# Kernel tuning notes

Hardware: AMD Instinct MI355X
Metric: run time of the kernel (lower is better)

Reference implementation:

```python
import jax, jax.numpy as jnp
import numpy as np

EPS_BN = 1e-5
EPS_LN = 1e-5

def _bn(x, g, b, m, v):
    # inference-mode BatchNorm2d over channel dim 1
    scale = g / jnp.sqrt(v + EPS_BN)
    return x * scale[None, :, None, None] + (b - m * scale)[None, :, None, None]

def _conv1x1(x, w, b=None):
    y = jnp.einsum('bchw,oc->bohw', x, w)
    if b is not None:
        y = y + b[None, :, None, None]
    return y

def _gelu(x):
    return jax.nn.gelu(x, approximate=False)

def setup_inputs() -> dict:
    key = jax.random.key(0)
    ks = jax.random.split(key, 40)
    B, C, H, W = 32, 160, 56, 56
    C5, C3 = C // 5, C * 3
    s = 0.05
    d = {}
    d['x'] = jax.random.normal(ks[0], (B, C, H, W), jnp.float32)
    d['bn1_g'] = jax.random.uniform(ks[1], (C,), jnp.float32, 0.5, 1.5)
    d['bn1_b'] = jax.random.normal(ks[2], (C,)) * s
    d['bn1_m'] = jax.random.normal(ks[3], (C,)) * s
    d['bn1_v'] = jnp.ones((C,), jnp.float32)
    names = ['t', 'b', 'r', 'l', 'c']
    for i, n in enumerate(names):
        d['w' + n] = jax.random.normal(ks[4 + i], (C5, C)) * s
        d['b' + n] = jax.random.normal(ks[9 + i], (C5,)) * s
    d['wf1'] = jax.random.normal(ks[14], (C, C)) * s
    d['bf1'] = jax.random.normal(ks[15], (C,)) * s
    d['bn2_g'] = jax.random.uniform(ks[16], (C,), jnp.float32, 0.5, 1.5)
    d['bn2_b'] = jax.random.normal(ks[17], (C,)) * s
    d['bn2_m'] = jax.random.normal(ks[18], (C,)) * s
    d['bn2_v'] = jnp.ones((C,), jnp.float32)
    d['wph'] = jax.random.normal(ks[19], (W, W)) * s
    d['bph'] = jax.random.normal(ks[20], (W,)) * s
    d['wpw'] = jax.random.normal(ks[21], (H, H)) * s
    d['bpw'] = jax.random.normal(ks[22], (H,)) * s
    d['wf2'] = jax.random.normal(ks[23], (C, C3)) * s
    d['ln_g'] = jax.random.uniform(ks[24], (C,), jnp.float32, 0.5, 1.5)
    d['ln_b'] = jax.random.normal(ks[25], (C,)) * s
    d['wfc1'] = jax.random.normal(ks[26], (C3, C)) * s
    d['bfc1'] = jax.random.normal(ks[27], (C3,)) * s
    d['wfc2'] = jax.random.normal(ks[28], (C, C3)) * s
    d['bfc2'] = jax.random.normal(ks[29], (C,)) * s
    d['step'] = 1
    return d

def reference(x, bn1_g, bn1_b, bn1_m, bn1_v, wt, bt, wb, bb, wr, br, wl, bl, wc, bc,
              wf1, bf1, bn2_g, bn2_b, bn2_m, bn2_v, wph, bph, wpw, bpw, wf2,
              ln_g, ln_b, wfc1, bfc1, wfc2, bfc2, step):
    B, C, H, W = x.shape
    # ---- localMix: ShiftedPillarsConcatentation_BNAct_NP5 ----
    h = _gelu(_bn(x, bn1_g, bn1_b, bn1_m, bn1_v))
    x_t = _conv1x1(h, wt, bt)
    x_b = _conv1x1(h, wb, bb)
    x_r = _conv1x1(h, wr, br)
    x_l = _conv1x1(h, wl, bl)
    x_c = _conv1x1(h, wc, bc)
    # pad then narrow exactly as torch: t/l shift by 1, b/r shift by step
    x_t = jnp.pad(x_t, ((0, 0), (0, 0), (0, step), (0, 0)))[:, :, 1:1 + H, :]
    x_b = jnp.pad(x_b, ((0, 0), (0, 0), (step, 0), (0, 0)))[:, :, 0:H, :]
    x_l = jnp.pad(x_l, ((0, 0), (0, 0), (0, 0), (0, step)))[:, :, :, 1:1 + W]
    x_r = jnp.pad(x_r, ((0, 0), (0, 0), (0, 0), (step, 0)))[:, :, :, 0:W]
    lm = _conv1x1(jnp.concatenate([x_t, x_b, x_r, x_l, x_c], axis=1), wf1, bf1)
    # ---- globalMix: sparseMLP_BNAct ----
    g = _gelu(_bn(lm, bn2_g, bn2_b, bn2_m, bn2_v))
    # proj_h mixes the W axis (input permuted to (B,W,C,H)), bias per output W
    x_h = jnp.einsum('bchw,vw->bchv', g, wph) + bph[None, None, None, :]
    # proj_w mixes the H axis (input permuted to (B,H,C,W)), bias per output H
    x_w = jnp.einsum('bchw,uh->bcuw', g, wpw) + bpw[None, None, :, None]
    gm = _conv1x1(jnp.concatenate([g, x_h, x_w], axis=1), wf2)  # no bias
    x1 = gm + x  # residual 1
    # ---- channelMix: LN + Mlp over channels ----
    y = jnp.transpose(x1, (0, 2, 3, 1))  # BHWC
    mu = jnp.mean(y, axis=-1, keepdims=True)
    var = jnp.mean(jnp.square(y - mu), axis=-1, keepdims=True)
    y = (y - mu) / jnp.sqrt(var + EPS_LN) * ln_g + ln_b
    y = _gelu(jnp.einsum('bhwc,fc->bhwf', y, wfc1) + bfc1)
    y = jnp.einsum('bhwf,cf->bhwc', y, wfc2) + bfc2
    return jnp.transpose(y, (0, 3, 1, 2)) + x1  # residual 2
```

## Files before the change

kernel.cpp:

```cpp
#include <hip/hip_runtime.h>
#include <hip/hip_bf16.h>
#include <math.h>

typedef __hip_bfloat16 bf16;
typedef __attribute__((ext_vector_type(8))) short s8v;
typedef __attribute__((ext_vector_type(4))) float f4v;

#define Bn  32
#define Cn  160
#define HWn 3136
#define Pn  100352

__device__ __forceinline__ float b2f(bf16 v){ return __bfloat162float(v); }
__device__ __forceinline__ bf16  f2b(float v){ return __float2bfloat16(v); }
__device__ __forceinline__ float bits2f(unsigned short u){
    union { float f; unsigned int i; } x; x.i = ((unsigned int)u) << 16; return x.f;
}
__device__ __forceinline__ float gelu_f(float x){ return 0.5f*x*(1.0f + erff(x*0.7071067811865476f)); }

#define MFMA(a,b,c) __builtin_amdgcn_mfma_f32_16x16x32_bf16((a),(b),(c),0,0,0)

__global__ __launch_bounds__(256) void k0_prep(
    const float* __restrict__ wt, const float* __restrict__ wb_, const float* __restrict__ wr,
    const float* __restrict__ wl, const float* __restrict__ wc,
    const float* __restrict__ bt, const float* __restrict__ bb_, const float* __restrict__ br,
    const float* __restrict__ bl, const float* __restrict__ bc,
    const float* __restrict__ wf1, const float* __restrict__ bf1,
    const float* __restrict__ g2, const float* __restrict__ b2, const float* __restrict__ m2, const float* __restrict__ v2,
    const float* __restrict__ wf2, const float* __restrict__ wfc1, const float* __restrict__ wfc2,
    const float* __restrict__ wph, const float* __restrict__ wpw,
    bf16* wcat, bf16* wf1b, bf16* wf2b, bf16* wfc1b, bf16* wfc2b, bf16* wphb, bf16* wpwb,
    float* bcat, float* epsv, float* eptv)
{
    int idx = blockIdx.x*256 + threadIdx.x;
    if (idx < 25600){ int o = idx/160, k = idx - o*160; int gi = o>>5, oo = o&31;
        const float* wp = gi==0?wt: gi==1?wb_: gi==2?wr: gi==3?wl: wc;
        wcat[idx] = f2b(wp[oo*160+k]); return; }
    idx -= 25600;
    if (idx < 25600){ wf1b[idx] = f2b(wf1[idx]); return; }
    idx -= 25600;
    if (idx < 76800){ wf2b[idx] = f2b(wf2[idx]); return; }
    idx -= 76800;
    if (idx < 76800){ wfc1b[idx] = f2b(wfc1[idx]); return; }
    idx -= 76800;
    if (idx < 76800){ wfc2b[idx] = f2b(wfc2[idx]); return; }
    idx -= 76800;
    if (idx < 4096){ int v = idx>>6, w = idx&63;
        wphb[idx] = (v<56 && w<56) ? f2b(wph[v*56+w]) : f2b(0.f); return; }
    idx -= 4096;
    if (idx < 4096){ int v = idx>>6, w = idx&63;
        wpwb[idx] = (v<56 && w<56) ? f2b(wpw[v*56+w]) : f2b(0.f); return; }
    idx -= 4096;
    if (idx < 160){ int o = idx; int gi = o>>5, oo = o&31;
        const float* bp = gi==0?bt: gi==1?bb_: gi==2?br: gi==3?bl: bc;
        bcat[o] = bp[oo]; return; }
    idx -= 160;
    if (idx < 160){ int o = idx; float s = g2[o]*rsqrtf(v2[o]+1e-5f);
        epsv[o] = s; eptv[o] = (bf1[o]-m2[o])*s + b2[o]; return; }
}

__global__ __launch_bounds__(256) void k1_bn_gelu_tr(const float* __restrict__ x,
    const float* __restrict__ g, const float* __restrict__ b,
    const float* __restrict__ m, const float* __restrict__ v,
    bf16* __restrict__ hT)
{
    __shared__ float tile[64*161];
    __shared__ float sc[160], sh[160];
    int blk = blockIdx.x; int bb = blk/49; int hw0 = (blk - bb*49)*64;
    int tid = threadIdx.x;
    if (tid < 160){
        float s = g[tid] * rsqrtf(v[tid] + 1e-5f);
        sc[tid] = s; sh[tid] = b[tid] - m[tid]*s;
    }
    __syncthreads();
    const float* xb = x + (size_t)bb*Cn*HWn + hw0;
    for (int idx = tid; idx < 160*64; idx += 256){
        int c = idx >> 6, p = idx & 63;
        float val = xb[(size_t)c*HWn + p];
        tile[p*161 + c] = gelu_f(val*sc[c] + sh[c]);
    }
    __syncthreads();
    bf16* ho = hT + ((size_t)bb*HWn + hw0)*Cn;
    for (int idx = tid; idx < 64*160; idx += 256){
        int p = idx/160, c = idx - p*160;
        ho[idx] = f2b(tile[p*161 + c]);
    }
}

__global__ __launch_bounds__(256) void k2_conv5(const bf16* __restrict__ hT,
    const bf16* __restrict__ wcat, const float* __restrict__ bcat, bf16* __restrict__ y5T)
{
    __shared__ __align__(16) unsigned short Bs[2][16*168];
    int tid = threadIdx.x, wave = tid>>6, lane = tid&63, m = lane&15, q = lane>>4;
    size_t pos0 = (size_t)blockIdx.x*64;
    const unsigned short* Ap = (const unsigned short*)hT + (pos0 + wave*16 + m)*160 + q*8;
    s8v a[5];
    #pragma unroll
    for (int kb = 0; kb < 5; ++kb) a[kb] = *(const s8v*)(Ap + kb*32);
    { const s8v* sp = (const s8v*)((const unsigned short*)wcat);
      for (int c = tid; c < 320; c += 256){ int row = c/20, col = (c - row*20)*8;
          *(s8v*)&Bs[0][row*168 + col] = sp[c]; } }
    __syncthreads();
    for (int s = 0; s < 10; ++s){
        if (s+1 < 10){
            const s8v* sp = (const s8v*)((const unsigned short*)wcat + (size_t)(s+1)*2560);
            for (int c = tid; c < 320; c += 256){ int row = c/20, col = (c - row*20)*8;
                *(s8v*)&Bs[(s+1)&1][row*168 + col] = sp[c]; }
        }
        f4v acc = {0.f,0.f,0.f,0.f};
        const unsigned short* Bp = &Bs[s&1][m*168 + q*8];
        #pragma unroll
        for (int kb = 0; kb < 5; ++kb) acc = MFMA(a[kb], *(const s8v*)(Bp + kb*32), acc);
        float bias = bcat[s*16 + m];
        bf16* yo = y5T + (pos0 + wave*16 + q*4)*160 + s*16 + m;
        #pragma unroll
        for (int r = 0; r < 4; ++r) yo[r*160] = f2b(acc[r] + bias);
        __syncthreads();
    }
}

__global__ __launch_bounds__(256) void k3_wf1(const bf16* __restrict__ y5T,
    const bf16* __restrict__ wf1b, const float* __restrict__ epsv, const float* __restrict__ eptv,
    bf16* __restrict__ gT)
{
    __shared__ __align__(16) unsigned short Bs[2][16*168];
    int tid = threadIdx.x, wave = tid>>6, lane = tid&63, m = lane&15, q = lane>>4;
    int blk = blockIdx.x; int bb = blk/49; int hw0 = (blk - bb*49)*64;
    size_t pos0 = (size_t)bb*HWn + hw0;
    int phw = hw0 + wave*16 + m; int h = phw/56, w = phw - h*56;
    s8v a[5];
    #pragma unroll
    for (int kb = 0; kb < 5; ++kb){
        int h2 = h, w2 = w; bool ok = true;
        if      (kb == 0){ h2 = h+1; ok = (h2 < 56); }
        else if (kb == 1){ h2 = h-1; ok = (h2 >= 0); }
        else if (kb == 2){ w2 = w-1; ok = (w2 >= 0); }
        else if (kb == 3){ w2 = w+1; ok = (w2 < 56); }
        if (ok){
            const unsigned short* Ap = (const unsigned short*)y5T +
                ((size_t)bb*HWn + h2*56 + w2)*160 + kb*32 + q*8;
            a[kb] = *(const s8v*)Ap;
        } else {
            a[kb] = (s8v){0,0,0,0,0,0,0,0};
        }
    }
    { const s8v* sp = (const s8v*)((const unsigned short*)wf1b);
      for (int c = tid; c < 320; c += 256){ int row = c/20, col = (c - row*20)*8;
          *(s8v*)&Bs[0][row*168 + col] = sp[c]; } }
    __syncthreads();
    for (int s = 0; s < 10; ++s){
        if (s+1 < 10){
            const s8v* sp = (const s8v*)((const unsigned short*)wf1b + (size_t)(s+1)*2560);
            for (int c = tid; c < 320; c += 256){ int row = c/20, col = (c - row*20)*8;
                *(s8v*)&Bs[(s+1)&1][row*168 + col] = sp[c]; }
        }
        f4v acc = {0.f,0.f,0.f,0.f};
        const unsigned short* Bp = &Bs[s&1][m*168 + q*8];
        #pragma unroll
        for (int kb = 0; kb < 5; ++kb) acc = MFMA(a[kb], *(const s8v*)(Bp + kb*32), acc);
        int o = s*16 + m;
        float es = epsv[o], et = eptv[o];
        bf16* go = gT + (pos0 + wave*16 + q*4)*160 + o;
        #pragma unroll
        for (int r = 0; r < 4; ++r) go[r*160] = f2b(gelu_f(acc[r]*es + et));
        __syncthreads();
    }
}

__global__ __launch_bounds__(256) void k4_projh(const bf16* __restrict__ gT,
    const bf16* __restrict__ wphb, const float* __restrict__ bph, bf16* __restrict__ xhT)
{
    __shared__ __align__(16) unsigned short gS[160*72];
    int tid = threadIdx.x, wave = tid>>6, lane = tid&63, m = lane&15, q = lane>>4;
    int blk = blockIdx.x; int b = blk/56, h = blk - b*56;
    const unsigned short* ga = (const unsigned short*)gT + ((size_t)b*HWn + h*56)*160;
    for (int idx = tid; idx < 56*160; idx += 256){
        int w = idx/160, c = idx - w*160;
        gS[c*72 + w] = ga[idx];
    }
    for (int idx = tid; idx < 160*8; idx += 256){
        int c = idx>>3, w = 56 + (idx&7);
        gS[c*72 + w] = 0;
    }
    __syncthreads();
    int v0 = wave*16;
    s8v a[2];
    #pragma unroll
    for (int kb = 0; kb < 2; ++kb)
        a[kb] = *(const s8v*)((const unsigned short*)wphb + (v0+m)*64 + kb*32 + q*8);
    int v = v0 + q*4;
    for (int s = 0; s < 10; ++s){
        f4v acc = {0.f,0.f,0.f,0.f};
        const unsigned short* Bp = &gS[(s*16+m)*72 + q*8];
        #pragma unroll
        for (int kb = 0; kb < 2; ++kb) acc = MFMA(a[kb], *(const s8v*)(Bp + kb*32), acc);
        #pragma unroll
        for (int r = 0; r < 4; ++r){
            int vv = v + r;
            if (vv < 56)
                xhT[((size_t)b*HWn + h*56 + vv)*160 + s*16 + m] = f2b(acc[r] + bph[vv]);
        }
    }
}

__global__ __launch_bounds__(256) void k5_projw(const bf16* __restrict__ gT,
    const bf16* __restrict__ wpwb, const float* __restrict__ bpw, bf16* __restrict__ xwT)
{
    __shared__ __align__(16) unsigned short gS[160*72];
    int tid = threadIdx.x, wave = tid>>6, lane = tid&63, m = lane&15, q = lane>>4;
    int blk = blockIdx.x; int b = blk/56, w = blk - b*56;
    const unsigned short* gbase = (const unsigned short*)gT + ((size_t)b*HWn + w)*160;
    for (int idx = tid; idx < 56*160; idx += 256){
        int hh = idx/160, c = idx - hh*160;
        gS[c*72 + hh] = gbase[(size_t)hh*56*160 + c];
    }
    for (int idx = tid; idx < 160*8; idx += 256){
        int c = idx>>3, hh = 56 + (idx&7);
        gS[c*72 + hh] = 0;
    }
    __syncthreads();
    int v0 = wave*16;
    s8v a[2];
    #pragma unroll
    for (int kb = 0; kb < 2; ++kb)
        a[kb] = *(const s8v*)((const unsigned short*)wpwb + (v0+m)*64 + kb*32 + q*8);
    int v = v0 + q*4;
    for (int s = 0; s < 10; ++s){
        f4v acc = {0.f,0.f,0.f,0.f};
        const unsigned short* Bp = &gS[(s*16+m)*72 + q*8];
        #pragma unroll
        for (int kb = 0; kb < 2; ++kb) acc = MFMA(a[kb], *(const s8v*)(Bp + kb*32), acc);
        #pragma unroll
        for (int r = 0; r < 4; ++r){
            int vv = v + r;
            if (vv < 56)
                xwT[((size_t)b*HWn + vv*56 + w)*160 + s*16 + m] = f2b(acc[r] + bpw[vv]);
        }
    }
}

__global__ __launch_bounds__(256) void k6_wf2(const bf16* __restrict__ gT,
    const bf16* __restrict__ xhT, const bf16* __restrict__ xwT,
    const bf16* __restrict__ wf2b, bf16* __restrict__ gm)
{
    __shared__ __align__(16) unsigned short Bs[2][16*488];
    int tid = threadIdx.x, wave = tid>>6, lane = tid&63, m = lane&15, q = lane>>4;
    size_t pos0 = (size_t)blockIdx.x*64;
    size_t prow = (pos0 + wave*16 + m)*160;
    s8v a[15];
    #pragma unroll
    for (int kb = 0; kb < 15; ++kb){
        const bf16* src = (kb < 5) ? gT : (kb < 10 ? xhT : xwT);
        int kc = (kb - (kb < 5 ? 0 : (kb < 10 ? 5 : 10)))*32 + q*8;
        a[kb] = *(const s8v*)((const unsigned short*)src + prow + kc);
    }
    { const s8v* sp = (const s8v*)((const unsigned short*)wf2b);
      for (int c = tid; c < 960; c += 256){ int row = c/60, col = (c - row*60)*8;
          *(s8v*)&Bs[0][row*488 + col] = sp[c]; } }
    __syncthreads();
    for (int s = 0; s < 10; ++s){
        if (s+1 < 10){
            const s8v* sp = (const s8v*)((const unsigned short*)wf2b + (size_t)(s+1)*7680);
            for (int c = tid; c < 960; c += 256){ int row = c/60, col = (c - row*60)*8;
                *(s8v*)&Bs[(s+1)&1][row*488 + col] = sp[c]; }
        }
        f4v acc = {0.f,0.f,0.f,0.f};
        const unsigned short* Bp = &Bs[s&1][m*488 + q*8];
        #pragma unroll
        for (int kb = 0; kb < 15; ++kb) acc = MFMA(a[kb], *(const s8v*)(Bp + kb*32), acc);
        bf16* go = gm + (pos0 + wave*16 + q*4)*160 + s*16 + m;
        #pragma unroll
        for (int r = 0; r < 4; ++r) go[r*160] = f2b(acc[r]);
        __syncthreads();
    }
}

__global__ __launch_bounds__(256) void k7_ln_fc1(const float* __restrict__ x,
    const bf16* __restrict__ gm,
    const float* __restrict__ lng, const float* __restrict__ lnb,
    const bf16* __restrict__ wfc1b, const float* __restrict__ bfc1, bf16* __restrict__ u)
{
    __shared__ float Xs[64*161];
    __shared__ __align__(16) unsigned short As[64*168];
    __shared__ __align__(16) unsigned short Bs[2][16*168];
    int tid = threadIdx.x, wave = tid>>6, lane = tid&63, m = lane&15, q = lane>>4;
    int blk = blockIdx.x; int bb = blk/49; int hw0 = (blk - bb*49)*64;
    size_t pos0 = (size_t)bb*HWn + hw0;
    const float* xb = x + (size_t)bb*Cn*HWn + hw0;
    for (int idx = tid; idx < 160*64; idx += 256){
        int o = idx >> 6, p = idx & 63;
        Xs[p*161 + o] = xb[(size_t)o*HWn + p];
    }
    { const s8v* sp = (const s8v*)((const unsigned short*)wfc1b);
      for (int c = tid; c < 320; c += 256){ int row = c/20, col = (c - row*20)*8;
          *(s8v*)&Bs[0][row*168 + col] = sp[c]; } }
    __syncthreads();
    {
        int p = tid >> 2, q4 = tid & 3;
        const unsigned short* gp = (const unsigned short*)gm + (pos0 + p)*160 + q4*40;
        float s = 0.f, ss = 0.f;
        #pragma unroll 8
        for (int i = 0; i < 40; ++i){
            int c = q4*40 + i;
            float vv = Xs[p*161 + c] + bits2f(gp[i]);
            Xs[p*161 + c] = vv;
            s += vv; ss += vv*vv;
        }
        s  += __shfl_xor(s, 1);  ss += __shfl_xor(ss, 1);
        s  += __shfl_xor(s, 2);  ss += __shfl_xor(ss, 2);
        float mean = s * (1.f/160.f);
        float var  = ss * (1.f/160.f) - mean*mean;
        float rstd = rsqrtf(var + 1e-5f);
        #pragma unroll 8
        for (int i = 0; i < 40; ++i){
            int c = q4*40 + i;
            float nv = (Xs[p*161 + c] - mean)*rstd*lng[c] + lnb[c];
            union { unsigned short us; bf16 b; } cv; cv.b = f2b(nv);
            As[p*168 + c] = cv.us;
        }
    }
    __syncthreads();
    s8v a[5];
    const unsigned short* Ap = &As[(wave*16 + m)*168 + q*8];
    #pragma unroll
    for (int kb = 0; kb < 5; ++kb) a[kb] = *(const s8v*)(Ap + kb*32);
    for (int s = 0; s < 30; ++s){
        if (s+1 < 30){
            const s8v* sp = (const s8v*)((const unsigned short*)wfc1b + (size_t)(s+1)*2560);
            for (int c = tid; c < 320; c += 256){ int row = c/20, col = (c - row*20)*8;
                *(s8v*)&Bs[(s+1)&1][row*168 + col] = sp[c]; }
        }
        f4v acc = {0.f,0.f,0.f,0.f};
        const unsigned short* Bp = &Bs[s&1][m*168 + q*8];
        #pragma unroll
        for (int kb = 0; kb < 5; ++kb) acc = MFMA(a[kb], *(const s8v*)(Bp + kb*32), acc);
        float bias = bfc1[s*16 + m];
        bf16* uo = u + (pos0 + wave*16 + q*4)*480 + s*16 + m;
        #pragma unroll
        for (int r = 0; r < 4; ++r) uo[r*480] = f2b(gelu_f(acc[r] + bias));
        __syncthreads();
    }
}

__global__ __launch_bounds__(256) void k8_fc2(const bf16* __restrict__ u,
    const bf16* __restrict__ wfc2b, const float* __restrict__ bfc2,
    const float* __restrict__ x, const bf16* __restrict__ gm, float* __restrict__ out)
{
    __shared__ float Ds[64*161];
    __shared__ __align__(16) unsigned short Bs[2][16*488];
    int tid = threadIdx.x, wave = tid>>6, lane = tid&63, m = lane&15, q = lane>>4;
    int blk = blockIdx.x; int bb = blk/49; int hw0 = (blk - bb*49)*64;
    size_t pos0 = (size_t)bb*HWn + hw0;
    const float* xb = x + (size_t)bb*Cn*HWn + hw0;
    for (int idx = tid; idx < 160*64; idx += 256){
        int o = idx >> 6, p = idx & 63;
        Ds[p*161 + o] = xb[(size_t)o*HWn + p];
    }
    { const s8v* sp = (const s8v*)((const unsigned short*)wfc2b);
      for (int c = tid; c < 960; c += 256){ int row = c/60, col = (c - row*60)*8;
          *(s8v*)&Bs[0][row*488 + col] = sp[c]; } }
    __syncthreads();
    {
        const unsigned short* gp = (const unsigned short*)gm + pos0*160;
        for (int idx = tid; idx < 64*160; idx += 256){
            int p = idx/160, c = idx - p*160;
            Ds[p*161 + c] += bits2f(gp[idx]);
        }
    }
    __syncthreads();
    const unsigned short* Ap = (const unsigned short*)u + (pos0 + wave*16 + m)*480 + q*8;
    s8v a[15];
    #pragma unroll
    for (int kb = 0; kb < 15; ++kb) a[kb] = *(const s8v*)(Ap + kb*32);
    for (int s = 0; s < 10; ++s){
        if (s+1 < 10){
            const s8v* sp = (const s8v*)((const unsigned short*)wfc2b + (size_t)(s+1)*7680);
            for (int c = tid; c < 960; c += 256){ int row = c/60, col = (c - row*60)*8;
                *(s8v*)&Bs[(s+1)&1][row*488 + col] = sp[c]; }
        }
        f4v acc = {0.f,0.f,0.f,0.f};
        const unsigned short* Bp = &Bs[s&1][m*488 + q*8];
        #pragma unroll
        for (int kb = 0; kb < 15; ++kb) acc = MFMA(a[kb], *(const s8v*)(Bp + kb*32), acc);
        int o = s*16 + m; float bias = bfc2[o];
        #pragma unroll
        for (int r = 0; r < 4; ++r)
            Ds[(wave*16 + q*4 + r)*161 + o] += acc[r] + bias;
        __syncthreads();
    }
    float* ob = out + (size_t)bb*Cn*HWn + hw0;
    for (int idx = tid; idx < 160*64; idx += 256){
        int o = idx >> 6, p = idx & 63;
        ob[(size_t)o*HWn + p] = Ds[p*161 + o];
    }
}

extern "C" void kernel_launch(void* const* d_in, const int* in_sizes, int n_in,
                              void* d_out, int out_size, void* d_ws, size_t ws_size,
                              hipStream_t stream)
{
    (void)in_sizes; (void)n_in; (void)out_size; (void)ws_size;
    const float* x     = (const float*)d_in[0];
    const float* bn1g  = (const float*)d_in[1];
    const float* bn1b  = (const float*)d_in[2];
    const float* bn1m  = (const float*)d_in[3];
    const float* bn1v  = (const float*)d_in[4];
    const float* wt    = (const float*)d_in[5];
    const float* bt    = (const float*)d_in[6];
    const float* wb    = (const float*)d_in[7];
    const float* bb    = (const float*)d_in[8];
    const float* wr    = (const float*)d_in[9];
    const float* br    = (const float*)d_in[10];
    const float* wl    = (const float*)d_in[11];
    const float* bl    = (const float*)d_in[12];
    const float* wc    = (const float*)d_in[13];
    const float* bc    = (const float*)d_in[14];
    const float* wf1   = (const float*)d_in[15];
    const float* bf1   = (const float*)d_in[16];
    const float* bn2g  = (const float*)d_in[17];
    const float* bn2b  = (const float*)d_in[18];
    const float* bn2m  = (const float*)d_in[19];
    const float* bn2v  = (const float*)d_in[20];
    const float* wph   = (const float*)d_in[21];
    const float* bph   = (const float*)d_in[22];
    const float* wpw   = (const float*)d_in[23];
    const float* bpw   = (const float*)d_in[24];
    const float* wf2   = (const float*)d_in[25];
    const float* lng   = (const float*)d_in[26];
    const float* lnb   = (const float*)d_in[27];
    const float* wfc1  = (const float*)d_in[28];
    const float* bfc1  = (const float*)d_in[29];
    const float* wfc2  = (const float*)d_in[30];
    const float* bfc2v = (const float*)d_in[31];
    float* outp = (float*)d_out;

    const size_t PC2 = (size_t)Pn*160*2;
    char* ws = (char*)d_ws;
    bf16* hT   = (bf16*)(ws + 0*PC2);
    bf16* y5T  = (bf16*)(ws + 1*PC2);
    bf16* gT   = (bf16*)(ws + 2*PC2);
    bf16* xhT  = (bf16*)(ws + 3*PC2);
    bf16* xwT  = (bf16*)(ws + 4*PC2);
    bf16* gm   = (bf16*)(ws + 5*PC2);
    char* wsw  = ws + 6*PC2;
    bf16*  wcat  = (bf16*)(wsw + 0);
    bf16*  wf1b  = (bf16*)(wsw + 51200);
    bf16*  wf2b  = (bf16*)(wsw + 102400);
    bf16*  wfc1b = (bf16*)(wsw + 256000);
    bf16*  wfc2b = (bf16*)(wsw + 409600);
    bf16*  wphb  = (bf16*)(wsw + 563200);
    bf16*  wpwb  = (bf16*)(wsw + 571392);
    float* bcat  = (float*)(wsw + 579584);
    float* epsv  = (float*)(wsw + 580224);
    float* eptv  = (float*)(wsw + 580864);
    bf16* uB   = (bf16*)(ws + 0);

    const int GP = Pn/64;
    const int GS = Bn*56;

    k0_prep<<<1134, 256, 0, stream>>>(wt, wb, wr, wl, wc, bt, bb, br, bl, bc,
                                      wf1, bf1, bn2g, bn2b, bn2m, bn2v,
                                      wf2, wfc1, wfc2, wph, wpw,
                                      wcat, wf1b, wf2b, wfc1b, wfc2b, wphb, wpwb,
                                      bcat, epsv, eptv);
    k1_bn_gelu_tr<<<GP, 256, 0, stream>>>(x, bn1g, bn1b, bn1m, bn1v, hT);
    k2_conv5     <<<GP, 256, 0, stream>>>(hT, wcat, bcat, y5T);
    k3_wf1       <<<GP, 256, 0, stream>>>(y5T, wf1b, epsv, eptv, gT);
    k4_projh     <<<GS, 256, 0, stream>>>(gT, wphb, bph, xhT);
    k5_projw     <<<GS, 256, 0, stream>>>(gT, wpwb, bpw, xwT);
    k6_wf2       <<<GP, 256, 0, stream>>>(gT, xhT, xwT, wf2b, gm);
    k7_ln_fc1    <<<GP, 256, 0, stream>>>(x, gm, lng, lnb, wfc1b, bfc1, uB);
    k8_fc2       <<<GP, 256, 0, stream>>>(uB, wfc2b, bfc2v, x, gm, outp);
}
```

Baseline: 562.0 us.

## Read GEMM weight fragments directly from global memory instead of LDS double-buffering

In the five channel-GEMM kernels (conv5, wf1, wf2, fc1, fc2), the shared-memory double-buffered weight staging and its per-step __syncthreads are removed. Each lane now loads its B-operand fragments straight from global memory, relying on L1/L2 caching because the small weight matrices are shared by all blocks. This removes LDS traffic and block-wide barriers per output tile and frees LDS for higher occupancy. In exchange there are more, possibly uncoalesced, global loads per wave. The LN kernel also adds the gm residual in a separate coalesced pass and keeps each row in registers for the normalize step.

Result: slower. 702.4 us (+25.0%).

```diff
diff --git a/kernel.cpp b/kernel.cpp
--- a/kernel.cpp
+++ b/kernel.cpp
@@ -90,32 +90,22 @@
 __global__ __launch_bounds__(256) void k2_conv5(const bf16* __restrict__ hT,
     const bf16* __restrict__ wcat, const float* __restrict__ bcat, bf16* __restrict__ y5T)
 {
-    __shared__ __align__(16) unsigned short Bs[2][16*168];
     int tid = threadIdx.x, wave = tid>>6, lane = tid&63, m = lane&15, q = lane>>4;
     size_t pos0 = (size_t)blockIdx.x*64;
     const unsigned short* Ap = (const unsigned short*)hT + (pos0 + wave*16 + m)*160 + q*8;
     s8v a[5];
     #pragma unroll
     for (int kb = 0; kb < 5; ++kb) a[kb] = *(const s8v*)(Ap + kb*32);
-    { const s8v* sp = (const s8v*)((const unsigned short*)wcat);
-      for (int c = tid; c < 320; c += 256){ int row = c/20, col = (c - row*20)*8;
-          *(s8v*)&Bs[0][row*168 + col] = sp[c]; } }
-    __syncthreads();
-    for (int s = 0; s < 10; ++s){
-        if (s+1 < 10){
-            const s8v* sp = (const s8v*)((const unsigned short*)wcat + (size_t)(s+1)*2560);
-            for (int c = tid; c < 320; c += 256){ int row = c/20, col = (c - row*20)*8;
-                *(s8v*)&Bs[(s+1)&1][row*168 + col] = sp[c]; }
-        }
-        f4v acc = {0.f,0.f,0.f,0.f};
-        const unsigned short* Bp = &Bs[s&1][m*168 + q*8];
+    const unsigned short* wbase = (const unsigned short*)wcat + m*160 + q*8;
+    for (int s = 0; s < 10; ++s){
+        const unsigned short* Bp = wbase + s*16*160;
+        f4v acc = {0.f,0.f,0.f,0.f};
         #pragma unroll
         for (int kb = 0; kb < 5; ++kb) acc = MFMA(a[kb], *(const s8v*)(Bp + kb*32), acc);
         float bias = bcat[s*16 + m];
         bf16* yo = y5T + (pos0 + wave*16 + q*4)*160 + s*16 + m;
         #pragma unroll
         for (int r = 0; r < 4; ++r) yo[r*160] = f2b(acc[r] + bias);
-        __syncthreads();
     }
 }
 
@@ -123,7 +113,6 @@
     const bf16* __restrict__ wf1b, const float* __restrict__ epsv, const float* __restrict__ eptv,
     bf16* __restrict__ gT)
 {
-    __shared__ __align__(16) unsigned short Bs[2][16*168];
     int tid = threadIdx.x, wave = tid>>6, lane = tid&63, m = lane&15, q = lane>>4;
     int blk = blockIdx.x; int bb = blk/49; int hw0 = (blk - bb*49)*64;
     size_t pos0 = (size_t)bb*HWn + hw0;
@@ -144,18 +133,10 @@
             a[kb] = (s8v){0,0,0,0,0,0,0,0};
         }
     }
-    { const s8v* sp = (const s8v*)((const unsigned short*)wf1b);
-      for (int c = tid; c < 320; c += 256){ int row = c/20, col = (c - row*20)*8;
-          *(s8v*)&Bs[0][row*168 + col] = sp[c]; } }
-    __syncthreads();
-    for (int s = 0; s < 10; ++s){
-        if (s+1 < 10){
-            const s8v* sp = (const s8v*)((const unsigned short*)wf1b + (size_t)(s+1)*2560);
-            for (int c = tid; c < 320; c += 256){ int row = c/20, col = (c - row*20)*8;
-                *(s8v*)&Bs[(s+1)&1][row*168 + col] = sp[c]; }
-        }
-        f4v acc = {0.f,0.f,0.f,0.f};
-        const unsigned short* Bp = &Bs[s&1][m*168 + q*8];
+    const unsigned short* wbase = (const unsigned short*)wf1b + m*160 + q*8;
+    for (int s = 0; s < 10; ++s){
+        const unsigned short* Bp = wbase + s*16*160;
+        f4v acc = {0.f,0.f,0.f,0.f};
         #pragma unroll
         for (int kb = 0; kb < 5; ++kb) acc = MFMA(a[kb], *(const s8v*)(Bp + kb*32), acc);
         int o = s*16 + m;
@@ -163,7 +144,6 @@
         bf16* go = gT + (pos0 + wave*16 + q*4)*160 + o;
         #pragma unroll
         for (int r = 0; r < 4; ++r) go[r*160] = f2b(gelu_f(acc[r]*es + et));
-        __syncthreads();
     }
 }
 
@@ -243,7 +223,6 @@
     const bf16* __restrict__ xhT, const bf16* __restrict__ xwT,
     const bf16* __restrict__ wf2b, bf16* __restrict__ gm)
 {
-    __shared__ __align__(16) unsigned short Bs[2][16*488];
     int tid = threadIdx.x, wave = tid>>6, lane = tid&63, m = lane&15, q = lane>>4;
     size_t pos0 = (size_t)blockIdx.x*64;
     size_t prow = (pos0 + wave*16 + m)*160;
@@ -254,24 +233,15 @@
         int kc = (kb - (kb < 5 ? 0 : (kb < 10 ? 5 : 10)))*32 + q*8;
         a[kb] = *(const s8v*)((const unsigned short*)src + prow + kc);
     }
-    { const s8v* sp = (const s8v*)((const unsigned short*)wf2b);
-      for (int c = tid; c < 960; c += 256){ int row = c/60, col = (c - row*60)*8;
-          *(s8v*)&Bs[0][row*488 + col] = sp[c]; } }
-    __syncthreads();
-    for (int s = 0; s < 10; ++s){
-        if (s+1 < 10){
-            const s8v* sp = (const s8v*)((const unsigned short*)wf2b + (size_t)(s+1)*7680);
-            for (int c = tid; c < 960; c += 256){ int row = c/60, col = (c - row*60)*8;
-                *(s8v*)&Bs[(s+1)&1][row*488 + col] = sp[c]; }
-        }
-        f4v acc = {0.f,0.f,0.f,0.f};
-        const unsigned short* Bp = &Bs[s&1][m*488 + q*8];
+    const unsigned short* wbase = (const unsigned short*)wf2b + m*480 + q*8;
+    for (int s = 0; s < 10; ++s){
+        const unsigned short* Bp = wbase + s*16*480;
+        f4v acc = {0.f,0.f,0.f,0.f};
         #pragma unroll
         for (int kb = 0; kb < 15; ++kb) acc = MFMA(a[kb], *(const s8v*)(Bp + kb*32), acc);
         bf16* go = gm + (pos0 + wave*16 + q*4)*160 + s*16 + m;
         #pragma unroll
         for (int r = 0; r < 4; ++r) go[r*160] = f2b(acc[r]);
-        __syncthreads();
     }
 }
 
@@ -282,7 +252,6 @@
 {
     __shared__ float Xs[64*161];
     __shared__ __align__(16) unsigned short As[64*168];
-    __shared__ __align__(16) unsigned short Bs[2][16*168];
     int tid = threadIdx.x, wave = tid>>6, lane = tid&63, m = lane&15, q = lane>>4;
     int blk = blockIdx.x; int bb = blk/49; int hw0 = (blk - bb*49)*64;
     size_t pos0 = (size_t)bb*HWn + hw0;
@@ -291,32 +260,34 @@
         int o = idx >> 6, p = idx & 63;
         Xs[p*161 + o] = xb[(size_t)o*HWn + p];
     }
-    { const s8v* sp = (const s8v*)((const unsigned short*)wfc1b);
-      for (int c = tid; c < 320; c += 256){ int row = c/20, col = (c - row*20)*8;
-          *(s8v*)&Bs[0][row*168 + col] = sp[c]; } }
+    __syncthreads();
+    {
+        const unsigned short* gp = (const unsigned short*)gm + pos0*160;
+        for (int idx = tid; idx < 64*160; idx += 256){
+            int p = idx/160, c = idx - p*160;
+            Xs[p*161 + c] += bits2f(gp[idx]);
+        }
+    }
     __syncthreads();
     {
         int p = tid >> 2, q4 = tid & 3;
-        const unsigned short* gp = (const unsigned short*)gm + (pos0 + p)*160 + q4*40;
+        float vbuf[40];
         float s = 0.f, ss = 0.f;
-        #pragma unroll 8
-        for (int i = 0; i < 40; ++i){
-            int c = q4*40 + i;
-            float vv = Xs[p*161 + c] + bits2f(gp[i]);
-            Xs[p*161 + c] = vv;
-            s += vv; ss += vv*vv;
-        }
+        const float* row = &Xs[p*161 + q4*40];
+        #pragma unroll
+        for (int i = 0; i < 40; ++i){ float vv = row[i]; vbuf[i] = vv; s += vv; ss += vv*vv; }
         s  += __shfl_xor(s, 1);  ss += __shfl_xor(ss, 1);
         s  += __shfl_xor(s, 2);  ss += __shfl_xor(ss, 2);
         float mean = s * (1.f/160.f);
         float var  = ss * (1.f/160.f) - mean*mean;
         float rstd = rsqrtf(var + 1e-5f);
-        #pragma unroll 8
+        unsigned short* arow = &As[p*168 + q4*40];
+        #pragma unroll
         for (int i = 0; i < 40; ++i){
             int c = q4*40 + i;
-            float nv = (Xs[p*161 + c] - mean)*rstd*lng[c] + lnb[c];
+            float nv = (vbuf[i] - mean)*rstd*lng[c] + lnb[c];
             union { unsigned short us; bf16 b; } cv; cv.b = f2b(nv);
-            As[p*168 + c] = cv.us;
+            arow[i] = cv.us;
         }
     }
     __syncthreads();
@@ -324,21 +295,16 @@
     const unsigned short* Ap = &As[(wave*16 + m)*168 + q*8];
     #pragma unroll
     for (int kb = 0; kb < 5; ++kb) a[kb] = *(const s8v*)(Ap + kb*32);
+    const unsigned short* wbase = (const unsigned short*)wfc1b + m*160 + q*8;
     for (int s = 0; s < 30; ++s){
-        if (s+1 < 30){
-            const s8v* sp = (const s8v*)((const unsigned short*)wfc1b + (size_t)(s+1)*2560);
-            for (int c = tid; c < 320; c += 256){ int row = c/20, col = (c - row*20)*8;
-                *(s8v*)&Bs[(s+1)&1][row*168 + col] = sp[c]; }
-        }
-        f4v acc = {0.f,0.f,0.f,0.f};
-        const unsigned short* Bp = &Bs[s&1][m*168 + q*8];
+        const unsigned short* Bp = wbase + s*16*160;
+        f4v acc = {0.f,0.f,0.f,0.f};
         #pragma unroll
         for (int kb = 0; kb < 5; ++kb) acc = MFMA(a[kb], *(const s8v*)(Bp + kb*32), acc);
         float bias = bfc1[s*16 + m];
         bf16* uo = u + (pos0 + wave*16 + q*4)*480 + s*16 + m;
         #pragma unroll
         for (int r = 0; r < 4; ++r) uo[r*480] = f2b(gelu_f(acc[r] + bias));
-        __syncthreads();
     }
 }
 
@@ -347,7 +313,6 @@
     const float* __restrict__ x, const bf16* __restrict__ gm, float* __restrict__ out)
 {
     __shared__ float Ds[64*161];
-    __shared__ __align__(16) unsigned short Bs[2][16*488];
     int tid = threadIdx.x, wave = tid>>6, lane = tid&63, m = lane&15, q = lane>>4;
     int blk = blockIdx.x; int bb = blk/49; int hw0 = (blk - bb*49)*64;
     size_t pos0 = (size_t)bb*HWn + hw0;
@@ -356,9 +321,6 @@
         int o = idx >> 6, p = idx & 63;
         Ds[p*161 + o] = xb[(size_t)o*HWn + p];
     }
-    { const s8v* sp = (const s8v*)((const unsigned short*)wfc2b);
-      for (int c = tid; c < 960; c += 256){ int row = c/60, col = (c - row*60)*8;
-          *(s8v*)&Bs[0][row*488 + col] = sp[c]; } }
     __syncthreads();
     {
         const unsigned short* gp = (const unsigned short*)gm + pos0*160;
@@ -372,22 +334,18 @@
     s8v a[15];
     #pragma unroll
     for (int kb = 0; kb < 15; ++kb) a[kb] = *(const s8v*)(Ap + kb*32);
-    for (int s = 0; s < 10; ++s){
-        if (s+1 < 10){
-            const s8v* sp = (const s8v*)((const unsigned short*)wfc2b + (size_t)(s+1)*7680);
-            for (int c = tid; c < 960; c += 256){ int row = c/60, col = (c - row*60)*8;
-                *(s8v*)&Bs[(s+1)&1][row*488 + col] = sp[c]; }
-        }
-        f4v acc = {0.f,0.f,0.f,0.f};
-        const unsigned short* Bp = &Bs[s&1][m*488 + q*8];
+    const unsigned short* wbase = (const unsigned short*)wfc2b + m*480 + q*8;
+    for (int s = 0; s < 10; ++s){
+        const unsigned short* Bp = wbase + s*16*480;
+        f4v acc = {0.f,0.f,0.f,0.f};
         #pragma unroll
         for (int kb = 0; kb < 15; ++kb) acc = MFMA(a[kb], *(const s8v*)(Bp + kb*32), acc);
         int o = s*16 + m; float bias = bfc2[o];
         #pragma unroll
         for (int r = 0; r < 4; ++r)
             Ds[(wave*16 + q*4 + r)*161 + o] += acc[r] + bias;
-        __syncthreads();
-    }
+    }
+    __syncthreads();
     float* ob = out + (size_t)bb*Cn*HWn + hw0;
     for (int idx = tid; idx < 160*64; idx += 256){
         int o = idx >> 6, p = idx & 63;
```
